# Kernel tuning notes

Measured on AMD Instinct MI355X. Metric: run time of the kernel, lower is better.

The kernel has to match this reference:

```python
import jax, jax.numpy as jnp
import numpy as np

NOISE_STD = 0.1
TOP_K = 2


def setup_inputs() -> dict:
    key = jax.random.key(0)
    k_x, k_n, k_w, k_keys = jax.random.split(key, 4)
    N, D_IN, D_Q, K = 16384, 2048, 256, 64
    x = jax.random.normal(k_x, (N, D_IN), dtype=jnp.float32)
    noise = jax.random.normal(k_n, (N, K), dtype=jnp.float32)
    # Linear params (kaiming-uniform-ish scale) and xavier-uniform keys
    w_q = jax.random.normal(k_w, (D_IN, D_Q), dtype=jnp.float32) * (1.0 / np.sqrt(D_IN))
    b_q = jnp.zeros((D_Q,), dtype=jnp.float32)
    lim = np.sqrt(6.0 / (K + D_Q))
    keys = jax.random.uniform(k_keys, (K, D_Q), dtype=jnp.float32, minval=-lim, maxval=lim)
    return {"x": x, "noise": noise, "w_q": w_q, "b_q": b_q, "keys": keys}


def reference(x, noise, w_q, b_q, keys):
    # query projection: [N, D_in] @ [D_in, D_q] -> [N, D_q]
    query = x @ w_q + b_q
    d_q = query.shape[-1]
    # router logits: [N, K], scaled dot product with expert keys
    logits = (query @ keys.T) * (1.0 / jnp.sqrt(jnp.asarray(d_q, query.dtype)))
    logits = logits + noise * NOISE_STD  # training-mode gating noise
    # top-k selection + softmax over selected logits only
    top_logits, top_idx = jax.lax.top_k(logits, TOP_K)       # [N, top_k]
    top_probs = jax.nn.softmax(top_logits, axis=-1)           # [N, top_k]
    # scatter selected probs into dense [N, K] gating tensor (zeros elsewhere)
    rows = jnp.arange(logits.shape[0])[:, None]               # [N, 1]
    gating_probs = jnp.zeros_like(logits).at[rows, top_idx].set(top_probs)
    return gating_probs, top_idx
```

## Files before the change

kernel.cpp:

```cpp
#include <hip/hip_runtime.h>

#define MROWS 16384
#define KD 2048
#define NQ 256
#define NE 64
#define INV_SQRT_DQ 0.0625f
#define NOISE_STD_C 0.1f

typedef _Float16 f16x8 __attribute__((ext_vector_type(8)));
typedef float f32x4 __attribute__((ext_vector_type(4)));

__device__ inline void split8v(f32x4 a, f32x4 b, f16x8* h, f16x8* l) {
    f16x8 hh, ll;
#pragma unroll
    for (int i = 0; i < 4; ++i) {
        _Float16 s = (_Float16)a[i];
        hh[i] = s; ll[i] = (_Float16)(a[i] - (float)s);
    }
#pragma unroll
    for (int i = 0; i < 4; ++i) {
        _Float16 s = (_Float16)b[i];
        hh[4 + i] = s; ll[4 + i] = (_Float16)(b[i] - (float)s);
    }
    *h = hh; *l = ll;
}

__global__ void prep_w(const float* __restrict__ w, _Float16* __restrict__ whp,
                       _Float16* __restrict__ wlp) {
    const int tid = blockIdx.x * 256 + threadIdx.x;
    const int f    = tid & 15;
    const int q    = (tid >> 4) & 3;
    const int ngrp = (tid >> 6) & 15;
    const int kcs  = tid >> 10;
    const int n = ngrp * 16 + f;
    const int k = kcs * 32 + q * 8;
    f16x8 h, l;
#pragma unroll
    for (int j = 0; j < 8; ++j) {
        float v = w[(size_t)(k + j) * NQ + n];
        _Float16 s = (_Float16)v;
        h[j] = s;
        l[j] = (_Float16)(v - (float)s);
    }
    *(f16x8*)(whp + (size_t)tid * 8) = h;
    *(f16x8*)(wlp + (size_t)tid * 8) = l;
}

__global__ __launch_bounds__(512) void gemm_fused(
    const float* __restrict__ x, const _Float16* __restrict__ whp,
    const _Float16* __restrict__ wlp, const float* __restrict__ bq,
    const float* __restrict__ keys, const float* __restrict__ noise,
    float* __restrict__ gate, float* __restrict__ idxout) {
    __shared__ __align__(16) char smem[66560];

    const int t = threadIdx.x;
    const int lane = t & 63;
    const int wv = t >> 6;
    const int m0 = blockIdx.x * 64;
    const int f = lane & 15;
    const int qq = lane >> 4;

    const int srow = t >> 4;
    const int soct = t & 15;
    const int swoff = (soct ^ (srow & 7)) * 8;
    const f32x4* xq0 = (const f32x4*)(x + (size_t)(m0 + srow) * KD + soct * 8);
    const f32x4* xq1 = (const f32x4*)(x + (size_t)(m0 + srow + 32) * KD + soct * 8);

    const _Float16* bph = whp + (size_t)(2 * wv) * 512 + lane * 8;
    const _Float16* bpl = wlp + (size_t)(2 * wv) * 512 + lane * 8;

    f32x4 acc[4][2];
#pragma unroll
    for (int mt = 0; mt < 4; ++mt)
#pragma unroll
        for (int nt = 0; nt < 2; ++nt) acc[mt][nt] = {0.f, 0.f, 0.f, 0.f};

    f32x4 a0 = __builtin_nontemporal_load(xq0);
    f32x4 a1 = __builtin_nontemporal_load(xq0 + 1);
    f32x4 b0 = __builtin_nontemporal_load(xq1);
    f32x4 b1 = __builtin_nontemporal_load(xq1 + 1);
    {
        _Float16* Ah = (_Float16*)smem;
        _Float16* Al = Ah + 8192;
        f16x8 h8, l8;
        split8v(a0, a1, &h8, &l8);
        *(f16x8*)(Ah + srow * 128 + swoff) = h8;
        *(f16x8*)(Al + srow * 128 + swoff) = l8;
        split8v(b0, b1, &h8, &l8);
        *(f16x8*)(Ah + (srow + 32) * 128 + swoff) = h8;
        *(f16x8*)(Al + (srow + 32) * 128 + swoff) = l8;
    }
    a0 = __builtin_nontemporal_load(xq0 + 32);
    a1 = __builtin_nontemporal_load(xq0 + 33);
    b0 = __builtin_nontemporal_load(xq1 + 32);
    b1 = __builtin_nontemporal_load(xq1 + 33);
    __syncthreads();

    f16x8 bh[2][2], bl[2][2];
#pragma unroll
    for (int nt = 0; nt < 2; ++nt) {
        bh[0][nt] = *(const f16x8*)(bph + nt * 512);
        bl[0][nt] = *(const f16x8*)(bpl + nt * 512);
    }

    for (int i = 0; i < 16; ++i) {
        _Float16* AhC = (_Float16*)smem + (i & 1) * 16384;
        _Float16* AlC = AhC + 8192;
        _Float16* AhN = (_Float16*)smem + ((i & 1) ^ 1) * 16384;
        _Float16* AlN = AhN + 8192;

        if (i < 15) {
            f16x8 h8, l8;
            split8v(a0, a1, &h8, &l8);
            *(f16x8*)(AhN + srow * 128 + swoff) = h8;
            *(f16x8*)(AlN + srow * 128 + swoff) = l8;
            split8v(b0, b1, &h8, &l8);
            *(f16x8*)(AhN + (srow + 32) * 128 + swoff) = h8;
            *(f16x8*)(AlN + (srow + 32) * 128 + swoff) = l8;
        }
        if (i < 14) {
            a0 = __builtin_nontemporal_load(xq0 + (i + 2) * 32);
            a1 = __builtin_nontemporal_load(xq0 + (i + 2) * 32 + 1);
            b0 = __builtin_nontemporal_load(xq1 + (i + 2) * 32);
            b1 = __builtin_nontemporal_load(xq1 + (i + 2) * 32 + 1);
        }
#pragma unroll
        for (int ks = 0; ks < 4; ++ks) {
            const int cs = ks & 1;
            const int ns = cs ^ 1;
            int kcn = i * 4 + ks + 1;
            if (kcn > 63) kcn = 63;
            const size_t bo = (size_t)kcn * 8192;
#pragma unroll
            for (int nt = 0; nt < 2; ++nt) {
                bh[ns][nt] = *(const f16x8*)(bph + bo + nt * 512);
                bl[ns][nt] = *(const f16x8*)(bpl + bo + nt * 512);
            }
            f16x8 ah[4], al[4];
#pragma unroll
            for (int mt = 0; mt < 4; ++mt) {
                const int ab = (mt * 16 + f) * 128 + (((ks * 4 + qq) ^ (f & 7)) * 8);
                ah[mt] = *(const f16x8*)(AhC + ab);
                al[mt] = *(const f16x8*)(AlC + ab);
            }
            __builtin_amdgcn_s_setprio(1);
#pragma unroll
            for (int mt = 0; mt < 4; ++mt)
#pragma unroll
                for (int nt = 0; nt < 2; ++nt) {
                    acc[mt][nt] = __builtin_amdgcn_mfma_f32_16x16x32_f16(ah[mt], bh[cs][nt], acc[mt][nt], 0, 0, 0);
                    acc[mt][nt] = __builtin_amdgcn_mfma_f32_16x16x32_f16(ah[mt], bl[cs][nt], acc[mt][nt], 0, 0, 0);
                    acc[mt][nt] = __builtin_amdgcn_mfma_f32_16x16x32_f16(al[mt], bh[cs][nt], acc[mt][nt], 0, 0, 0);
                }
            __builtin_amdgcn_s_setprio(0);
        }
        asm volatile("" ::: "memory");
        __builtin_amdgcn_s_waitcnt(0xC07F);
        __builtin_amdgcn_s_barrier();
        asm volatile("" ::: "memory");
    }

    float* qs = (float*)smem;
#pragma unroll
    for (int nt = 0; nt < 2; ++nt) {
        int col = wv * 32 + nt * 16 + f;
        float bias = bq[col];
#pragma unroll
        for (int mt = 0; mt < 4; ++mt)
#pragma unroll
            for (int r = 0; r < 4; ++r)
                qs[(mt * 16 + qq * 4 + r) * 260 + col] = acc[mt][nt][r] + bias;
    }
    __syncthreads();

    const int e = wv * 16 + f;
    f32x4 a2[4];
#pragma unroll
    for (int mt = 0; mt < 4; ++mt) a2[mt] = {0.f, 0.f, 0.f, 0.f};
    if (wv < 4) {
        const float* kp = keys + (size_t)e * NQ + qq * 8;
        for (int kc = 0; kc < NQ; kc += 32) {
            f32x4 k0 = *(const f32x4*)(kp + kc);
            f32x4 k1 = *(const f32x4*)(kp + kc + 4);
            f16x8 bh2, bl2;
            split8v(k0, k1, &bh2, &bl2);
#pragma unroll
            for (int mt = 0; mt < 4; ++mt) {
                const float* ap = qs + (mt * 16 + f) * 260 + kc + qq * 8;
                f32x4 q0 = *(const f32x4*)ap;
                f32x4 q1 = *(const f32x4*)(ap + 4);
                f16x8 ah2, al2;
                split8v(q0, q1, &ah2, &al2);
                a2[mt] = __builtin_amdgcn_mfma_f32_16x16x32_f16(ah2, bh2, a2[mt], 0, 0, 0);
                a2[mt] = __builtin_amdgcn_mfma_f32_16x16x32_f16(ah2, bl2, a2[mt], 0, 0, 0);
                a2[mt] = __builtin_amdgcn_mfma_f32_16x16x32_f16(al2, bh2, a2[mt], 0, 0, 0);
            }
        }
    }
    __syncthreads();

    float* LG = (float*)smem;
    if (wv < 4) {
#pragma unroll
        for (int mt = 0; mt < 4; ++mt)
#pragma unroll
            for (int r = 0; r < 4; ++r) {
                int row = mt * 16 + qq * 4 + r;
                LG[row * 65 + e] = a2[mt][r] * INV_SQRT_DQ +
                                   NOISE_STD_C * noise[(size_t)(m0 + row) * NE + e];
            }
    }
    __syncthreads();

    for (int i = 0; i < 8; ++i) {
        int r = wv * 8 + i;
        float v = LG[r * 65 + lane];
        float v1 = v; int i1 = lane;
#pragma unroll
        for (int off = 32; off; off >>= 1) {
            float ov = __shfl_xor(v1, off);
            int oi = __shfl_xor(i1, off);
            if (ov > v1 || (ov == v1 && oi < i1)) { v1 = ov; i1 = oi; }
        }
        float v2 = (lane == i1) ? -1e30f : v;
        int i2 = lane;
#pragma unroll
        for (int off = 32; off; off >>= 1) {
            float ov = __shfl_xor(v2, off);
            int oi = __shfl_xor(i2, off);
            if (ov > v2 || (ov == v2 && oi < i2)) { v2 = ov; i2 = oi; }
        }
        float ex = expf(v2 - v1);
        float p1 = 1.0f / (1.0f + ex);
        float p2 = ex * p1;
        float g = (lane == i1) ? p1 : ((lane == i2) ? p2 : 0.0f);
        gate[(size_t)(m0 + r) * NE + lane] = g;
        if (lane == 0) {
            float2 ii = make_float2((float)i1, (float)i2);
            *(float2*)(idxout + (size_t)(m0 + r) * 2) = ii;
        }
    }
}

extern "C" void kernel_launch(void* const* d_in, const int* in_sizes, int n_in,
                              void* d_out, int out_size, void* d_ws, size_t ws_size,
                              hipStream_t stream) {
    const float* x     = (const float*)d_in[0];
    const float* noise = (const float*)d_in[1];
    const float* w_q   = (const float*)d_in[2];
    const float* b_q   = (const float*)d_in[3];
    const float* keys  = (const float*)d_in[4];
    float* out = (float*)d_out;

    char* ws = (char*)d_ws;
    _Float16* whp = (_Float16*)ws;
    _Float16* wlp = (_Float16*)(ws + (1u << 20));

    prep_w<<<256, 256, 0, stream>>>(w_q, whp, wlp);
    gemm_fused<<<256, 512, 0, stream>>>(x, whp, wlp, b_q, keys, noise,
                                        out, out + (size_t)MROWS * NE);
}
```

Measured before the change: 233.3 us.

## Fold query projection and expert keys into a single combined weight matrix

Precomputes W_q·keys^T (and the bias·keys term) in a prep kernel using double accumulation, so the main fused kernel does a 2048x64 GEMM instead of 2048x256 followed by a second GEMM. This removes most of the split-fp16 MFMA work and the shared-memory query staging. The prep kernel now does a sizeable FP64 reduction on few blocks, and rounding behavior changes because the logits are formed from a precombined weight.

New measurement: 252.4 us. 1.08x slower.

```diff
diff --git a/kernel.cpp b/kernel.cpp
--- a/kernel.cpp
+++ b/kernel.cpp
@@ -25,37 +25,61 @@
     *h = hh; *l = ll;
 }
 
-__global__ void prep_w(const float* __restrict__ w, _Float16* __restrict__ whp,
-                       _Float16* __restrict__ wlp) {
+__global__ __launch_bounds__(256) void prep_w2(
+    const float* __restrict__ w, const float* __restrict__ keys,
+    const float* __restrict__ bq, _Float16* __restrict__ whp,
+    _Float16* __restrict__ wlp, float* __restrict__ css) {
     const int tid = blockIdx.x * 256 + threadIdx.x;
-    const int f    = tid & 15;
-    const int q    = (tid >> 4) & 3;
-    const int ngrp = (tid >> 6) & 15;
-    const int kcs  = tid >> 10;
-    const int n = ngrp * 16 + f;
-    const int k = kcs * 32 + q * 8;
+    const int e = tid & 63;
+    const int o = tid >> 6;
+    const float* kp = keys + (size_t)e * NQ;
+    const float* wp = w + (size_t)o * 8 * NQ;
+    double acc[8];
+#pragma unroll
+    for (int j = 0; j < 8; ++j) acc[j] = 0.0;
+    for (int q = 0; q < NQ; q += 4) {
+        f32x4 kv = *(const f32x4*)(kp + q);
+#pragma unroll
+        for (int j = 0; j < 8; ++j) {
+            f32x4 wv = *(const f32x4*)(wp + (size_t)j * NQ + q);
+#pragma unroll
+            for (int u = 0; u < 4; ++u)
+                acc[j] += (double)wv[u] * (double)kv[u];
+        }
+    }
+    const int kc32 = o >> 2;
+    const int qqp  = o & 3;
+    const size_t base = ((size_t)kc32 * 4 + (e >> 4)) * 512 + (size_t)(qqp * 16 + (e & 15)) * 8;
     f16x8 h, l;
 #pragma unroll
     for (int j = 0; j < 8; ++j) {
-        float v = w[(size_t)(k + j) * NQ + n];
+        float v = (float)acc[j];
         _Float16 s = (_Float16)v;
         h[j] = s;
         l[j] = (_Float16)(v - (float)s);
     }
-    *(f16x8*)(whp + (size_t)tid * 8) = h;
-    *(f16x8*)(wlp + (size_t)tid * 8) = l;
-}
-
-__global__ __launch_bounds__(512) void gemm_fused(
+    *(f16x8*)(whp + base) = h;
+    *(f16x8*)(wlp + base) = l;
+    if (blockIdx.x == 0 && threadIdx.x < NE) {
+        const float* kp2 = keys + (size_t)threadIdx.x * NQ;
+        double s = 0.0;
+        for (int q = 0; q < NQ; ++q) s += (double)bq[q] * (double)kp2[q];
+        css[threadIdx.x] = (float)(s * 0.0625);
+    }
+}
+
+__global__ __launch_bounds__(512) void gemm2_fused(
     const float* __restrict__ x, const _Float16* __restrict__ whp,
-    const _Float16* __restrict__ wlp, const float* __restrict__ bq,
-    const float* __restrict__ keys, const float* __restrict__ noise,
-    float* __restrict__ gate, float* __restrict__ idxout) {
-    __shared__ __align__(16) char smem[66560];
+    const _Float16* __restrict__ wlp, const float* __restrict__ css,
+    const float* __restrict__ noise, float* __restrict__ gate,
+    float* __restrict__ idxout) {
+    __shared__ __align__(16) char smem[65536];
 
     const int t = threadIdx.x;
     const int lane = t & 63;
     const int wv = t >> 6;
+    const int wn = wv & 3;
+    const int wm = wv >> 2;
     const int m0 = blockIdx.x * 64;
     const int f = lane & 15;
     const int qq = lane >> 4;
@@ -66,14 +90,12 @@
     const f32x4* xq0 = (const f32x4*)(x + (size_t)(m0 + srow) * KD + soct * 8);
     const f32x4* xq1 = (const f32x4*)(x + (size_t)(m0 + srow + 32) * KD + soct * 8);
 
-    const _Float16* bph = whp + (size_t)(2 * wv) * 512 + lane * 8;
-    const _Float16* bpl = wlp + (size_t)(2 * wv) * 512 + lane * 8;
-
-    f32x4 acc[4][2];
-#pragma unroll
-    for (int mt = 0; mt < 4; ++mt)
-#pragma unroll
-        for (int nt = 0; nt < 2; ++nt) acc[mt][nt] = {0.f, 0.f, 0.f, 0.f};
+    const _Float16* bph = whp + (size_t)wn * 512 + lane * 8;
+    const _Float16* bpl = wlp + (size_t)wn * 512 + lane * 8;
+
+    f32x4 acc[2];
+    acc[0] = {0.f, 0.f, 0.f, 0.f};
+    acc[1] = {0.f, 0.f, 0.f, 0.f};
 
     f32x4 a0 = __builtin_nontemporal_load(xq0);
     f32x4 a1 = __builtin_nontemporal_load(xq0 + 1);
@@ -96,11 +118,11 @@
     b1 = __builtin_nontemporal_load(xq1 + 33);
     __syncthreads();
 
-    f16x8 bh[2][2], bl[2][2];
-#pragma unroll
-    for (int nt = 0; nt < 2; ++nt) {
-        bh[0][nt] = *(const f16x8*)(bph + nt * 512);
-        bl[0][nt] = *(const f16x8*)(bpl + nt * 512);
+    f16x8 bhS[4], blS[4];
+#pragma unroll
+    for (int ks = 0; ks < 4; ++ks) {
+        bhS[ks] = *(const f16x8*)(bph + (size_t)ks * 2048);
+        blS[ks] = *(const f16x8*)(bpl + (size_t)ks * 2048);
     }
 
     for (int i = 0; i < 16; ++i) {
@@ -126,33 +148,24 @@
         }
 #pragma unroll
         for (int ks = 0; ks < 4; ++ks) {
-            const int cs = ks & 1;
-            const int ns = cs ^ 1;
-            int kcn = i * 4 + ks + 1;
-            if (kcn > 63) kcn = 63;
-            const size_t bo = (size_t)kcn * 8192;
-#pragma unroll
-            for (int nt = 0; nt < 2; ++nt) {
-                bh[ns][nt] = *(const f16x8*)(bph + bo + nt * 512);
-                bl[ns][nt] = *(const f16x8*)(bpl + bo + nt * 512);
-            }
-            f16x8 ah[4], al[4];
-#pragma unroll
-            for (int mt = 0; mt < 4; ++mt) {
-                const int ab = (mt * 16 + f) * 128 + (((ks * 4 + qq) ^ (f & 7)) * 8);
+            f16x8 ah[2], al[2];
+#pragma unroll
+            for (int mt = 0; mt < 2; ++mt) {
+                const int row = (wm * 2 + mt) * 16 + f;
+                const int ab = row * 128 + (((ks * 4 + qq) ^ (row & 7)) * 8);
                 ah[mt] = *(const f16x8*)(AhC + ab);
                 al[mt] = *(const f16x8*)(AlC + ab);
             }
-            __builtin_amdgcn_s_setprio(1);
-#pragma unroll
-            for (int mt = 0; mt < 4; ++mt)
-#pragma unroll
-                for (int nt = 0; nt < 2; ++nt) {
-                    acc[mt][nt] = __builtin_amdgcn_mfma_f32_16x16x32_f16(ah[mt], bh[cs][nt], acc[mt][nt], 0, 0, 0);
-                    acc[mt][nt] = __builtin_amdgcn_mfma_f32_16x16x32_f16(ah[mt], bl[cs][nt], acc[mt][nt], 0, 0, 0);
-                    acc[mt][nt] = __builtin_amdgcn_mfma_f32_16x16x32_f16(al[mt], bh[cs][nt], acc[mt][nt], 0, 0, 0);
-                }
-            __builtin_amdgcn_s_setprio(0);
+#pragma unroll
+            for (int mt = 0; mt < 2; ++mt) {
+                acc[mt] = __builtin_amdgcn_mfma_f32_16x16x32_f16(ah[mt], bhS[ks], acc[mt], 0, 0, 0);
+                acc[mt] = __builtin_amdgcn_mfma_f32_16x16x32_f16(ah[mt], blS[ks], acc[mt], 0, 0, 0);
+                acc[mt] = __builtin_amdgcn_mfma_f32_16x16x32_f16(al[mt], bhS[ks], acc[mt], 0, 0, 0);
+            }
+            int gn = i * 4 + ks + 4;
+            if (gn > 63) gn = 63;
+            bhS[ks] = *(const f16x8*)(bph + (size_t)gn * 2048);
+            blS[ks] = *(const f16x8*)(bpl + (size_t)gn * 2048);
         }
         asm volatile("" ::: "memory");
         __builtin_amdgcn_s_waitcnt(0xC07F);
@@ -160,56 +173,17 @@
         asm volatile("" ::: "memory");
     }
 
-    float* qs = (float*)smem;
-#pragma unroll
-    for (int nt = 0; nt < 2; ++nt) {
-        int col = wv * 32 + nt * 16 + f;
-        float bias = bq[col];
-#pragma unroll
-        for (int mt = 0; mt < 4; ++mt)
-#pragma unroll
-            for (int r = 0; r < 4; ++r)
-                qs[(mt * 16 + qq * 4 + r) * 260 + col] = acc[mt][nt][r] + bias;
-    }
-    __syncthreads();
-
-    const int e = wv * 16 + f;
-    f32x4 a2[4];
-#pragma unroll
-    for (int mt = 0; mt < 4; ++mt) a2[mt] = {0.f, 0.f, 0.f, 0.f};
-    if (wv < 4) {
-        const float* kp = keys + (size_t)e * NQ + qq * 8;
-        for (int kc = 0; kc < NQ; kc += 32) {
-            f32x4 k0 = *(const f32x4*)(kp + kc);
-            f32x4 k1 = *(const f32x4*)(kp + kc + 4);
-            f16x8 bh2, bl2;
-            split8v(k0, k1, &bh2, &bl2);
-#pragma unroll
-            for (int mt = 0; mt < 4; ++mt) {
-                const float* ap = qs + (mt * 16 + f) * 260 + kc + qq * 8;
-                f32x4 q0 = *(const f32x4*)ap;
-                f32x4 q1 = *(const f32x4*)(ap + 4);
-                f16x8 ah2, al2;
-                split8v(q0, q1, &ah2, &al2);
-                a2[mt] = __builtin_amdgcn_mfma_f32_16x16x32_f16(ah2, bh2, a2[mt], 0, 0, 0);
-                a2[mt] = __builtin_amdgcn_mfma_f32_16x16x32_f16(ah2, bl2, a2[mt], 0, 0, 0);
-                a2[mt] = __builtin_amdgcn_mfma_f32_16x16x32_f16(al2, bh2, a2[mt], 0, 0, 0);
-            }
-        }
-    }
-    __syncthreads();
-
     float* LG = (float*)smem;
-    if (wv < 4) {
-#pragma unroll
-        for (int mt = 0; mt < 4; ++mt)
-#pragma unroll
-            for (int r = 0; r < 4; ++r) {
-                int row = mt * 16 + qq * 4 + r;
-                LG[row * 65 + e] = a2[mt][r] * INV_SQRT_DQ +
-                                   NOISE_STD_C * noise[(size_t)(m0 + row) * NE + e];
-            }
-    }
+    const int e = wn * 16 + f;
+    const float cse = css[e];
+#pragma unroll
+    for (int mt = 0; mt < 2; ++mt)
+#pragma unroll
+        for (int r = 0; r < 4; ++r) {
+            int row = (wm * 2 + mt) * 16 + qq * 4 + r;
+            LG[row * 65 + e] = acc[mt][r] * INV_SQRT_DQ + cse +
+                               NOISE_STD_C * noise[(size_t)(m0 + row) * NE + e];
+        }
     __syncthreads();
 
     for (int i = 0; i < 8; ++i) {
@@ -254,9 +228,10 @@
 
     char* ws = (char*)d_ws;
     _Float16* whp = (_Float16*)ws;
-    _Float16* wlp = (_Float16*)(ws + (1u << 20));
-
-    prep_w<<<256, 256, 0, stream>>>(w_q, whp, wlp);
-    gemm_fused<<<256, 512, 0, stream>>>(x, whp, wlp, b_q, keys, noise,
-                                        out, out + (size_t)MROWS * NE);
-}
+    _Float16* wlp = (_Float16*)(ws + (256u << 10));
+    float* css    = (float*)(ws + (512u << 10));
+
+    prep_w2<<<64, 256, 0, stream>>>(w_q, keys, b_q, whp, wlp, css);
+    gemm2_fused<<<256, 512, 0, stream>>>(x, whp, wlp, css, noise,
+                                         out, out + (size_t)MROWS * NE);
+}
```
